# Optimization experiments

Measured on AMD Instinct MI355X. Metric: run time of the kernel, lower is better.

Reference implementation:

```python
import jax, jax.numpy as jnp
import numpy as np

B, S, D = 2, 2048, 2048
NQ, NKV = 32, 8
HD = D // NQ  # 64
THETA = 10000.0


def _rope_tables(seq_len, head_dim, theta):
    k = jnp.arange(0, head_dim, 2)[: head_dim // 2].astype(jnp.float32)
    inv_freq = 1.0 / (theta ** (k / head_dim))
    pos = jnp.arange(seq_len, dtype=jnp.float32)
    ang = pos[:, None] * inv_freq[None, :]          # [S, HD/2]
    ang = jnp.concatenate([ang, ang], axis=-1)       # [S, HD]
    return jnp.cos(ang), jnp.sin(ang)


def _apply_rope(x, cos, sin):
    # x: [B, H, S, HD]; cos/sin: [S, HD]
    h = x.shape[-1] // 2
    x1, x2 = x[..., :h], x[..., h:]
    rotated = jnp.concatenate([-x2, x1], axis=-1)
    return (x * cos[None, None] + rotated * sin[None, None]).astype(x.dtype)


def setup_inputs() -> dict:
    key = jax.random.key(0)
    ks = jax.random.split(key, 6)
    x = jax.random.normal(ks[0], (B, S, D), dtype=jnp.float32)
    attention_mask = jnp.ones((B, S), dtype=jnp.int32)
    Wq = jax.random.normal(ks[1], (NQ * HD, D), dtype=jnp.float32) * 0.02
    Wk = jax.random.normal(ks[2], (NKV * HD, D), dtype=jnp.float32) * 0.02
    Wv = jax.random.normal(ks[3], (NKV * HD, D), dtype=jnp.float32) * 0.02
    Wo = jax.random.normal(ks[4], (D, D), dtype=jnp.float32) * 0.02
    return {"x": x, "attention_mask": attention_mask,
            "Wq": Wq, "Wk": Wk, "Wv": Wv, "Wo": Wo}


def reference(x, attention_mask, Wq, Wk, Wv, Wo):
    b, s, d = x.shape
    # projections (nn.Linear: y = x @ W.T)
    q = jnp.einsum('bsd,od->bso', x, Wq).reshape(b, s, NQ, HD).transpose(0, 2, 1, 3)
    k = jnp.einsum('bsd,od->bso', x, Wk).reshape(b, s, NKV, HD).transpose(0, 2, 1, 3)
    v = jnp.einsum('bsd,od->bso', x, Wv).reshape(b, s, NKV, HD).transpose(0, 2, 1, 3)
    cos, sin = _rope_tables(s, HD, THETA)
    q = _apply_rope(q, cos, sin)
    k = _apply_rope(k, cos, sin)
    g = NQ // NKV
    k = jnp.repeat(k, g, axis=1)  # [b, NQ, s, HD]
    v = jnp.repeat(v, g, axis=1)
    attn = jnp.einsum('bhqd,bhkd->bhqk', q, k)
    causal = jnp.triu(jnp.ones((s, s), dtype=bool), k=1)
    attn = jnp.where(causal[None, None], -jnp.inf, attn)
    attn = jax.nn.softmax(attn / jnp.sqrt(jnp.float32(HD)), axis=-1)
    out = jnp.einsum('bhqk,bhkd->bhqd', attn, v)
    out = out.transpose(0, 2, 1, 3).reshape(b, s, d)
    return jnp.einsum('bsd,od->bso', out, Wo)
```

## Files before the change

### kernel.cpp

```cpp
#include <hip/hip_runtime.h>

#define B_   2
#define S_   2048
#define D_   2048
#define NQ_  32
#define NKV_ 8
#define HD_  64

typedef unsigned short u16;
typedef __bf16 bf16x8 __attribute__((ext_vector_type(8)));
typedef __bf16 bf16x4 __attribute__((ext_vector_type(4)));
typedef short  s16x4  __attribute__((ext_vector_type(4)));
typedef float  f32x4  __attribute__((ext_vector_type(4)));

#define GLB __attribute__((address_space(1)))
#define LDS __attribute__((address_space(3)))

__device__ inline u16 f2b(float f){
  union { float f; unsigned u; } v; v.f = f;
  unsigned r = (v.u + 0x7fffu + ((v.u >> 16) & 1u)) >> 16;
  return (u16)r;
}
__device__ inline float b2f(u16 b){
  union { unsigned u; float f; } v; v.u = ((unsigned)b) << 16;
  return v.f;
}

__device__ inline f32x4 mfma16(bf16x4 a, bf16x4 b, f32x4 c){
  union U { bf16x4 b; s16x4 s; };
  U ua, ub; ua.b = a; ub.b = b;
  return __builtin_amdgcn_mfma_f32_16x16x16bf16_1k(ua.s, ub.s, c, 0, 0, 0);
}

__device__ inline bf16x4 pack4(float p0, float p1, float p2, float p3){
  union { float f; unsigned u; } a, b, c, d;
  a.f = p0; b.f = p1; c.f = p2; d.f = p3;
  union { uint2 u; bf16x4 v; } r;
  r.u.x = (a.u >> 16) | (b.u & 0xffff0000u);
  r.u.y = (c.u >> 16) | (d.u & 0xffff0000u);
  return r.v;
}

__global__ void k_f2b_all(const float* __restrict__ x,  const float* __restrict__ wq,
                          const float* __restrict__ wk, const float* __restrict__ wv,
                          const float* __restrict__ wo,
                          u16* __restrict__ xb, u16* __restrict__ wqkvb, u16* __restrict__ wob){
  int i = blockIdx.x * blockDim.x + threadIdx.x;
  const float* src; u16* dst; int off;
  if (i < 2097152)      { src = x;  dst = xb;                  off = i; }
  else if (i < 3145728) { src = wq; dst = wqkvb;               off = i - 2097152; }
  else if (i < 3407872) { src = wk; dst = wqkvb + 2048*2048;   off = i - 3145728; }
  else if (i < 3670016) { src = wv; dst = wqkvb + 2560*2048;   off = i - 3407872; }
  else                  { src = wo; dst = wob;                 off = i - 3670016; }
  float4 f = ((const float4*)src)[off];
  uint2 pk;
  pk.x = (unsigned)f2b(f.x) | ((unsigned)f2b(f.y) << 16);
  pk.y = (unsigned)f2b(f.z) | ((unsigned)f2b(f.w) << 16);
  ((uint2*)dst)[off] = pk;
}

#define GEMM_CORE(K)                                                           \
  __shared__ __align__(16) u16 As[128*64];                                     \
  __shared__ __align__(16) u16 Bs[128*64];                                     \
  const int tid  = threadIdx.x;                                               \
  const int lane = tid & 63;                                                  \
  const int wave = tid >> 6;                                                  \
  const int wm = wave >> 1, wn = wave & 1;                                    \
  const int quad = lane >> 4, l16 = lane & 15;                                \
  const u16* Ab = A  + (size_t)blockIdx.y * 128 * (K);                        \
  const u16* Bb = Bm + (size_t)blockIdx.x * 128 * (K);                        \
  f32x4 acc[4][4];                                                            \
  for (int i = 0; i < 4; i++)                                                 \
    for (int j = 0; j < 4; j++) acc[i][j] = (f32x4){0.f, 0.f, 0.f, 0.f};      \
  const int R0 = wave * 32;                                                   \
  const int lr = lane >> 3;                                                   \
  const int gc = ((lane & 7) ^ lr) * 8;                                       \
  const int sk = l16 & 7;                                                     \
  for (int k0 = 0; k0 < (K); k0 += 64){                                       \
    __syncthreads();                                                          \
    _Pragma("unroll")                                                         \
    for (int m = 0; m < 4; m++){                                              \
      const u16* ga = Ab + (size_t)(R0 + m*8 + lr) * (K) + k0 + gc;           \
      const u16* gb = Bb + (size_t)(R0 + m*8 + lr) * (K) + k0 + gc;           \
      __builtin_amdgcn_global_load_lds((const GLB void*)ga, (LDS void*)&As[(R0 + m*8)*64], 16, 0, 0); \
      __builtin_amdgcn_global_load_lds((const GLB void*)gb, (LDS void*)&Bs[(R0 + m*8)*64], 16, 0, 0); \
    }                                                                          \
    __syncthreads();                                                          \
    bf16x8 af[4][2], bfr[4][2];                                               \
    _Pragma("unroll")                                                         \
    for (int i = 0; i < 4; i++)                                               \
      _Pragma("unroll")                                                       \
      for (int h = 0; h < 2; h++)                                             \
        af[i][h]  = *(const bf16x8*)&As[(wm*64 + i*16 + l16)*64 + (((h*4 + quad) ^ sk)*8)]; \
    _Pragma("unroll")                                                         \
    for (int j = 0; j < 4; j++)                                               \
      _Pragma("unroll")                                                       \
      for (int h = 0; h < 2; h++)                                             \
        bfr[j][h] = *(const bf16x8*)&Bs[(wn*64 + j*16 + l16)*64 + (((h*4 + quad) ^ sk)*8)]; \
    _Pragma("unroll")                                                         \
    for (int i = 0; i < 4; i++)                                               \
      _Pragma("unroll")                                                       \
      for (int j = 0; j < 4; j++){                                            \
        acc[i][j] = __builtin_amdgcn_mfma_f32_16x16x32_bf16(af[i][0], bfr[j][0], acc[i][j], 0, 0, 0); \
        acc[i][j] = __builtin_amdgcn_mfma_f32_16x16x32_bf16(af[i][1], bfr[j][1], acc[i][j], 0, 0, 0); \
      }                                                                        \
  }

#define QSCALE 0.18033688011112042f
__global__ __launch_bounds__(256, 3) void k_gemm_qkv(const u16* __restrict__ A,
                                                     const u16* __restrict__ Bm,
                                                     u16* __restrict__ qT,
                                                     u16* __restrict__ kT,
                                                     u16* __restrict__ vT){
  GEMM_CORE(2048)

  const int cb = blockIdx.x*128 + wn*64;

  if (cb < 2560){
    const bool isq = (cb < 2048);
    const int hh   = (isq ? cb : (cb - 2048)) >> 6;
    const int NH   = isq ? NQ_ : NKV_;
    u16* base      = isq ? qT : kT;
    const float sc = isq ? QSCALE : 1.0f;
    #pragma unroll
    for (int j = 0; j < 2; j++){
      const int d2 = j*16 + l16;
      const float invf = __expf(-(float)d2 * (9.210340371976184f / 32.0f));
      #pragma unroll
      for (int i = 0; i < 4; i++){
        const int row0 = blockIdx.y*128 + wm*64 + i*16 + quad*4;
        #pragma unroll
        for (int r = 0; r < 4; r++){
          const int row = row0 + r;
          const int s = row & (S_ - 1), b = row >> 11;
          float ang = (float)s * invf;
          float sn = __sinf(ang), cs = __cosf(ang);
          const float x1 = acc[i][j][r] * sc, x2 = acc[i][j+2][r] * sc;
          u16* drow = base + ((size_t)(b*NH + hh) * S_ + s) * 64;
          drow[d2]      = f2b(x1*cs - x2*sn);
          drow[d2 + 32] = f2b(x2*cs + x1*sn);
        }
      }
    }
  } else {
    const int fbase = cb - 2560;
    #pragma unroll
    for (int j = 0; j < 4; j++){
      const int f = fbase + j*16 + l16;
      const int kvh = f >> 6, d = f & 63;
      #pragma unroll
      for (int i = 0; i < 4; i++){
        const int row0 = blockIdx.y*128 + wm*64 + i*16 + quad*4;
        const int s0 = row0 & (S_ - 1), b = row0 >> 11;
        uint2 pk;
        pk.x = (unsigned)f2b(acc[i][j][0]) | ((unsigned)f2b(acc[i][j][1]) << 16);
        pk.y = (unsigned)f2b(acc[i][j][2]) | ((unsigned)f2b(acc[i][j][3]) << 16);
        *(uint2*)(vT + ((size_t)(b*NKV_ + kvh) * 64 + d) * S_ + s0) = pk;
      }
    }
  }
}

__global__ __launch_bounds__(256, 3) void k_gemm_bt(const u16* __restrict__ A,
                                                    const u16* __restrict__ Bm,
                                                    float* __restrict__ C,
                                                    int N){
  GEMM_CORE(2048)
  for (int i = 0; i < 4; i++){
    int row0 = blockIdx.y*128 + wm*64 + i*16 + quad*4;
    for (int j = 0; j < 4; j++){
      int col = blockIdx.x*128 + wn*64 + j*16 + l16;
      for (int r = 0; r < 4; r++)
        C[(size_t)(row0 + r) * N + col] = acc[i][j][r];
    }
  }
}

__global__ __launch_bounds__(256) void k_attn(const u16* __restrict__ qT,
                                              const u16* __restrict__ kT,
                                              const u16* __restrict__ vT,
                                              u16* __restrict__ P1,
                                              u16* __restrict__ P2,
                                              float* __restrict__ l1,
                                              float* __restrict__ l2){
  __shared__ __align__(16) u16 Ks[2][64*64];
  __shared__ __align__(16) u16 Vs[2][64*64];

  const int bid  = blockIdx.x;
  const int kvh  = bid & 7;
  const int b    = (bid >> 3) & 1;
  const int hq   = (bid >> 4) & 3;
  const int p    = (bid >> 6) & 7;
  const int half = bid >> 9;
  const int h    = kvh*4 + hq;
  const int lane = threadIdx.x & 63, w = threadIdx.x >> 6;
  const int quad = lane >> 4, l16 = lane & 15;

  const u16* Qh = qT + (size_t)(b*NQ_ + h)    * S_ * 64;
  const u16* Kh = kT + (size_t)(b*NKV_ + kvh) * S_ * 64;
  const u16* Vh = vT + (size_t)(b*NKV_ + kvh) * 64 * S_;

  const int rr = lane >> 3;
  const int gg = (lane & 7) ^ rr;
  const int R  = w * 16;

  auto stage = [&](int c, int buf){
    const int kb = c * 64;
    const u16* gk0 = Kh + (size_t)(kb + R + rr)     * 64 + gg*8;
    const u16* gk1 = Kh + (size_t)(kb + R + 8 + rr) * 64 + gg*8;
    const u16* gv0 = Vh + (size_t)(R + rr)     * S_ + kb + gg*8;
    const u16* gv1 = Vh + (size_t)(R + 8 + rr) * S_ + kb + gg*8;
    __builtin_amdgcn_global_load_lds((const GLB void*)gk0, (LDS void*)&Ks[buf][R*64],     16, 0, 0);
    __builtin_amdgcn_global_load_lds((const GLB void*)gk1, (LDS void*)&Ks[buf][(R+8)*64], 16, 0, 0);
    __builtin_amdgcn_global_load_lds((const GLB void*)gv0, (LDS void*)&Vs[buf][R*64],     16, 0, 0);
    __builtin_amdgcn_global_load_lds((const GLB void*)gv1, (LDS void*)&Vs[buf][(R+8)*64], 16, 0, 0);
  };

  const int sw    = l16 & 7;
  const int koff0 = ((quad    ) ^ sw) * 8;
  const int koff1 = ((quad + 4) ^ sw) * 8;
  int voff[4];
  #pragma unroll
  for (int t = 0; t < 4; t++)
    voff[t] = (((2*t + (quad >> 1)) ^ sw) * 8) + (quad & 1)*4;

  for (int ph = 0; ph < 2; ph++){
    int tile, c0, c1, slot;
    if (ph == 0){ tile = p;
      if (half == 0){ c0 = 0;      c1 = p + 1;     slot = 0; }
      else          { c0 = p + 1;  c1 = 2*p + 2;   slot = 1; }
    } else {      tile = 15 - p;
      if (half == 0){ c0 = 16 - p; c1 = 32 - 2*p;  slot = 1; }
      else          { c0 = 0;      c1 = 16 - p;    slot = 0; }
    }
    const int qb0 = 2*tile, qb1 = 2*tile + 1;
    const int qr0 = tile*128 + w*16 + l16;
    const int qr1 = qr0 + 64;
    const int nc  = c1 - c0;

    if (ph == 1) __syncthreads();
    stage(c0, 0);

    bf16x8 qf[2][2];
    qf[0][0] = *(const bf16x8*)(Qh + (size_t)qr0*64 + quad*8);
    qf[0][1] = *(const bf16x8*)(Qh + (size_t)qr0*64 + 32 + quad*8);
    qf[1][0] = *(const bf16x8*)(Qh + (size_t)qr1*64 + quad*8);
    qf[1][1] = *(const bf16x8*)(Qh + (size_t)qr1*64 + 32 + quad*8);

    f32x4 o[2][4];
    #pragma unroll
    for (int s = 0; s < 2; s++)
      for (int dt = 0; dt < 4; dt++) o[s][dt] = (f32x4){0.f, 0.f, 0.f, 0.f};
    float lrow[2] = {0.f, 0.f};

    for (int i = 0; i < nc; i++){
      const int c = c0 + i;
      const int buf = i & 1;
      __syncthreads();
      if (i + 1 < nc) stage(c + 1, buf^1);

      const bool act0  = (c <= qb0);
      const bool diag0 = (c == qb0);
      const bool diag1 = (c == qb1);
      const u16* Kb = &Ks[buf][0];
      const u16* Vb = &Vs[buf][0];

      bf16x4 pk[2][4];
      #pragma unroll
      for (int t = 0; t < 4; t++){
        const bool n0 = act0 && !(diag0 && t > w);
        const bool n1 = !(diag1 && t > w);
        if (!n0 && !n1) continue;
        const int rowb = (t*16 + l16)*64;
        bf16x8 ka0 = *(const bf16x8*)&Kb[rowb + koff0];
        bf16x8 ka1 = *(const bf16x8*)&Kb[rowb + koff1];
        #pragma unroll
        for (int s = 0; s < 2; s++){
          if (s == 0 ? !n0 : !n1) continue;
          f32x4 z = (f32x4){0.f, 0.f, 0.f, 0.f};
          z = __builtin_amdgcn_mfma_f32_16x16x32_bf16(ka0, qf[s][0], z, 0, 0, 0);
          z = __builtin_amdgcn_mfma_f32_16x16x32_bf16(ka1, qf[s][1], z, 0, 0, 0);
          if ((s == 0 ? diag0 : diag1) && t == w){
            #pragma unroll
            for (int r = 0; r < 4; r++)
              if (quad*4 + r > l16) z[r] = -1e30f;
          }
          float p0 = __builtin_amdgcn_exp2f(z[0]);
          float p1 = __builtin_amdgcn_exp2f(z[1]);
          float p2 = __builtin_amdgcn_exp2f(z[2]);
          float p3 = __builtin_amdgcn_exp2f(z[3]);
          lrow[s] += (p0 + p1) + (p2 + p3);
          pk[s][t] = pack4(p0, p1, p2, p3);
        }
      }

      #pragma unroll
      for (int dt = 0; dt < 4; dt++){
        const int rowb = (dt*16 + l16)*64;
        #pragma unroll
        for (int t = 0; t < 4; t++){
          const bool n0 = act0 && !(diag0 && t > w);
          const bool n1 = !(diag1 && t > w);
          if (!n0 && !n1) continue;
          bf16x4 va = *(const bf16x4*)&Vb[rowb + voff[t]];
          if (n0) o[0][dt] = mfma16(va, pk[0][t], o[0][dt]);
          if (n1) o[1][dt] = mfma16(va, pk[1][t], o[1][dt]);
        }
      }
    }

    u16*   Pd = slot ? P2 : P1;
    float* ld = slot ? l2 : l1;
    #pragma unroll
    for (int s = 0; s < 2; s++){
      float lsum = lrow[s];
      lsum += __shfl_xor(lsum, 16, 64);
      lsum += __shfl_xor(lsum, 32, 64);
      const int qrow = s ? qr1 : qr0;
      if (quad == 0) ld[(size_t)(b*S_ + qrow)*NQ_ + h] = lsum;
      u16* orow = Pd + (size_t)(b*S_ + qrow) * D_ + h*64;
      #pragma unroll
      for (int dt = 0; dt < 4; dt++){
        uint2 pkd;
        u16 e0 = f2b(o[s][dt][0]), e1 = f2b(o[s][dt][1]);
        u16 e2 = f2b(o[s][dt][2]), e3 = f2b(o[s][dt][3]);
        pkd.x = (unsigned)e0 | ((unsigned)e1 << 16);
        pkd.y = (unsigned)e2 | ((unsigned)e3 << 16);
        *(uint2*)(orow + dt*16 + quad*4) = pkd;
      }
    }
  }
}

__global__ void k_combine(const u16* __restrict__ P1, const u16* __restrict__ P2,
                          const float* __restrict__ l1, const float* __restrict__ l2,
                          u16* __restrict__ out){
  int i = blockIdx.x * blockDim.x + threadIdx.x;
  int e = i << 2;
  int li = (e >> 11)*NQ_ + ((e >> 6) & 31);
  float inv = 1.0f / (l1[li] + l2[li]);
  uint2 a = *(const uint2*)(P1 + e);
  uint2 bq = *(const uint2*)(P2 + e);
  float o0 = (b2f(a.x & 0xffff)  + b2f(bq.x & 0xffff))  * inv;
  float o1 = (b2f(a.x >> 16)     + b2f(bq.x >> 16))     * inv;
  float o2 = (b2f(a.y & 0xffff)  + b2f(bq.y & 0xffff))  * inv;
  float o3 = (b2f(a.y >> 16)     + b2f(bq.y >> 16))     * inv;
  uint2 pk;
  pk.x = (unsigned)f2b(o0) | ((unsigned)f2b(o1) << 16);
  pk.y = (unsigned)f2b(o2) | ((unsigned)f2b(o3) << 16);
  *(uint2*)(out + e) = pk;
}

extern "C" void kernel_launch(void* const* d_in, const int* in_sizes, int n_in,
                              void* d_out, int out_size, void* d_ws, size_t ws_size,
                              hipStream_t stream){
  const float* x  = (const float*)d_in[0];
  const float* Wq = (const float*)d_in[2];
  const float* Wk = (const float*)d_in[3];
  const float* Wv = (const float*)d_in[4];
  const float* Wo = (const float*)d_in[5];

  char* ws = (char*)d_ws;
  u16*   xb    = (u16*)(ws);
  u16*   wqkvb = (u16*)(ws + 16777216);
  u16*   wob   = (u16*)(ws + 29360128);
  u16*   qTp   = (u16*)(ws + 37748736);
  u16*   kTp   = (u16*)(ws + 54525952);
  u16*   vTp   = (u16*)(ws + 58720256);
  u16*   P1    = xb;
  u16*   P2    = (u16*)(ws + 62914560);
  float* l1    = (float*)(ws + 79691776);
  float* l2    = (float*)(ws + 80216064);
  u16*   attnOut = qTp;

  k_f2b_all<<<dim3(18432), 256, 0, stream>>>(x, Wq, Wk, Wv, Wo, xb, wqkvb, wob);

  k_gemm_qkv<<<dim3(24, 32), 256, 0, stream>>>(xb, wqkvb, qTp, kTp, vTp);

  k_attn<<<dim3(1024), 256, 0, stream>>>(qTp, kTp, vTp, P1, P2, l1, l2);

  k_combine<<<dim3(8192), 256, 0, stream>>>(P1, P2, l1, l2, attnOut);

  k_gemm_bt<<<dim3(16, 32), 256, 0, stream>>>(attnOut, wob, (float*)d_out, 2048);
}
```

Before: 309.7 us.

## Split attention into one tile per block with heaviest tiles first

The attention kernel used to pair a light and a heavy query tile inside each of 1024 blocks, each block running two phases. It now launches 2048 blocks, and each block handles a single 128-row query tile and one half of its causal key range. Block indices are ordered so the longest tiles (T=15 down to 0) are scheduled first, which should give a longest-first load balance and more blocks to fill the CUs. The V-offset precompute is moved inline and the bf16x4 type is replaced by s16x4 to drop the union casts. The cost is a Q-fragment reload and output write per block, and more blocks with short work at the tail.

```diff
diff --git a/kernel.cpp b/kernel.cpp
--- a/kernel.cpp
+++ b/kernel.cpp
@@ -9,7 +9,6 @@
 
 typedef unsigned short u16;
 typedef __bf16 bf16x8 __attribute__((ext_vector_type(8)));
-typedef __bf16 bf16x4 __attribute__((ext_vector_type(4)));
 typedef short  s16x4  __attribute__((ext_vector_type(4)));
 typedef float  f32x4  __attribute__((ext_vector_type(4)));
 
@@ -26,16 +25,14 @@
   return v.f;
 }
 
-__device__ inline f32x4 mfma16(bf16x4 a, bf16x4 b, f32x4 c){
-  union U { bf16x4 b; s16x4 s; };
-  U ua, ub; ua.b = a; ub.b = b;
-  return __builtin_amdgcn_mfma_f32_16x16x16bf16_1k(ua.s, ub.s, c, 0, 0, 0);
-}
-
-__device__ inline bf16x4 pack4(float p0, float p1, float p2, float p3){
+__device__ inline f32x4 mfma16(s16x4 a, s16x4 b, f32x4 c){
+  return __builtin_amdgcn_mfma_f32_16x16x16bf16_1k(a, b, c, 0, 0, 0);
+}
+
+__device__ inline s16x4 pack4(float p0, float p1, float p2, float p3){
   union { float f; unsigned u; } a, b, c, d;
   a.f = p0; b.f = p1; c.f = p2; d.f = p3;
-  union { uint2 u; bf16x4 v; } r;
+  union { uint2 u; s16x4 v; } r;
   r.u.x = (a.u >> 16) | (b.u & 0xffff0000u);
   r.u.y = (c.u >> 16) | (d.u & 0xffff0000u);
   return r.v;
@@ -190,8 +187,9 @@
   const int kvh  = bid & 7;
   const int b    = (bid >> 3) & 1;
   const int hq   = (bid >> 4) & 3;
-  const int p    = (bid >> 6) & 7;
-  const int half = bid >> 9;
+  const int j    = bid >> 6;
+  const int T    = 15 - (j >> 1);
+  const int half = j & 1;
   const int h    = kvh*4 + hq;
   const int lane = threadIdx.x & 63, w = threadIdx.x >> 6;
   const int quad = lane >> 4, l16 = lane & 15;
@@ -219,115 +217,102 @@
   const int sw    = l16 & 7;
   const int koff0 = ((quad    ) ^ sw) * 8;
   const int koff1 = ((quad + 4) ^ sw) * 8;
-  int voff[4];
+
+  const int qb0 = 2*T, qb1 = 2*T + 1;
+  const int qr0 = T*128 + w*16 + l16;
+  const int qr1 = qr0 + 64;
+  const int c0  = half ? (T + 1) : 0;
+  const int nc  = T + 1;
+
+  stage(c0, 0);
+
+  bf16x8 qf[2][2];
+  qf[0][0] = *(const bf16x8*)(Qh + (size_t)qr0*64 + quad*8);
+  qf[0][1] = *(const bf16x8*)(Qh + (size_t)qr0*64 + 32 + quad*8);
+  qf[1][0] = *(const bf16x8*)(Qh + (size_t)qr1*64 + quad*8);
+  qf[1][1] = *(const bf16x8*)(Qh + (size_t)qr1*64 + 32 + quad*8);
+
+  f32x4 o[2][4];
   #pragma unroll
-  for (int t = 0; t < 4; t++)
-    voff[t] = (((2*t + (quad >> 1)) ^ sw) * 8) + (quad & 1)*4;
-
-  for (int ph = 0; ph < 2; ph++){
-    int tile, c0, c1, slot;
-    if (ph == 0){ tile = p;
-      if (half == 0){ c0 = 0;      c1 = p + 1;     slot = 0; }
-      else          { c0 = p + 1;  c1 = 2*p + 2;   slot = 1; }
-    } else {      tile = 15 - p;
-      if (half == 0){ c0 = 16 - p; c1 = 32 - 2*p;  slot = 1; }
-      else          { c0 = 0;      c1 = 16 - p;    slot = 0; }
-    }
-    const int qb0 = 2*tile, qb1 = 2*tile + 1;
-    const int qr0 = tile*128 + w*16 + l16;
-    const int qr1 = qr0 + 64;
-    const int nc  = c1 - c0;
-
-    if (ph == 1) __syncthreads();
-    stage(c0, 0);
-
-    bf16x8 qf[2][2];
-    qf[0][0] = *(const bf16x8*)(Qh + (size_t)qr0*64 + quad*8);
-    qf[0][1] = *(const bf16x8*)(Qh + (size_t)qr0*64 + 32 + quad*8);
-    qf[1][0] = *(const bf16x8*)(Qh + (size_t)qr1*64 + quad*8);
-    qf[1][1] = *(const bf16x8*)(Qh + (size_t)qr1*64 + 32 + quad*8);
-
-    f32x4 o[2][4];
-    #pragma unroll
-    for (int s = 0; s < 2; s++)
-      for (int dt = 0; dt < 4; dt++) o[s][dt] = (f32x4){0.f, 0.f, 0.f, 0.f};
-    float lrow[2] = {0.f, 0.f};
-
-    for (int i = 0; i < nc; i++){
-      const int c = c0 + i;
-      const int buf = i & 1;
-      __syncthreads();
-      if (i + 1 < nc) stage(c + 1, buf^1);
-
-      const bool act0  = (c <= qb0);
-      const bool diag0 = (c == qb0);
-      const bool diag1 = (c == qb1);
-      const u16* Kb = &Ks[buf][0];
-      const u16* Vb = &Vs[buf][0];
-
-      bf16x4 pk[2][4];
+  for (int s = 0; s < 2; s++)
+    for (int dt = 0; dt < 4; dt++) o[s][dt] = (f32x4){0.f, 0.f, 0.f, 0.f};
+  float lrow[2] = {0.f, 0.f};
+
+  for (int i = 0; i < nc; i++){
+    const int c = c0 + i;
+    const int buf = i & 1;
+    __syncthreads();
+    if (i + 1 < nc) stage(c + 1, buf^1);
+
+    const bool act0  = (c <= qb0);
+    const bool diag0 = (c == qb0);
+    const bool diag1 = (c == qb1);
+    const u16* Kb = &Ks[buf][0];
+    const u16* Vb = &Vs[buf][0];
+
+    s16x4 pk[2][4];
+    #pragma unroll
+    for (int t = 0; t < 4; t++){
+      const bool n0 = act0 && !(diag0 && t > w);
+      const bool n1 = !(diag1 && t > w);
+      if (!n0 && !n1) continue;
+      const int rowb = (t*16 + l16)*64;
+      bf16x8 ka0 = *(const bf16x8*)&Kb[rowb + koff0];
+      bf16x8 ka1 = *(const bf16x8*)&Kb[rowb + koff1];
+      #pragma unroll
+      for (int s = 0; s < 2; s++){
+        if (s == 0 ? !n0 : !n1) continue;
+        f32x4 z = (f32x4){0.f, 0.f, 0.f, 0.f};
+        z = __builtin_amdgcn_mfma_f32_16x16x32_bf16(ka0, qf[s][0], z, 0, 0, 0);
+        z = __builtin_amdgcn_mfma_f32_16x16x32_bf16(ka1, qf[s][1], z, 0, 0, 0);
+        if ((s == 0 ? diag0 : diag1) && t == w){
+          #pragma unroll
+          for (int r = 0; r < 4; r++)
+            if (quad*4 + r > l16) z[r] = -1e30f;
+        }
+        float p0 = __builtin_amdgcn_exp2f(z[0]);
+        float p1 = __builtin_amdgcn_exp2f(z[1]);
+        float p2 = __builtin_amdgcn_exp2f(z[2]);
+        float p3 = __builtin_amdgcn_exp2f(z[3]);
+        lrow[s] += (p0 + p1) + (p2 + p3);
+        pk[s][t] = pack4(p0, p1, p2, p3);
+      }
+    }
+
+    #pragma unroll
+    for (int dt = 0; dt < 4; dt++){
+      const int rowb = (dt*16 + l16)*64;
       #pragma unroll
       for (int t = 0; t < 4; t++){
         const bool n0 = act0 && !(diag0 && t > w);
         const bool n1 = !(diag1 && t > w);
         if (!n0 && !n1) continue;
-        const int rowb = (t*16 + l16)*64;
-        bf16x8 ka0 = *(const bf16x8*)&Kb[rowb + koff0];
-        bf16x8 ka1 = *(const bf16x8*)&Kb[rowb + koff1];
-        #pragma unroll
-        for (int s = 0; s < 2; s++){
-          if (s == 0 ? !n0 : !n1) continue;
-          f32x4 z = (f32x4){0.f, 0.f, 0.f, 0.f};
-          z = __builtin_amdgcn_mfma_f32_16x16x32_bf16(ka0, qf[s][0], z, 0, 0, 0);
-          z = __builtin_amdgcn_mfma_f32_16x16x32_bf16(ka1, qf[s][1], z, 0, 0, 0);
-          if ((s == 0 ? diag0 : diag1) && t == w){
-            #pragma unroll
-            for (int r = 0; r < 4; r++)
-              if (quad*4 + r > l16) z[r] = -1e30f;
-          }
-          float p0 = __builtin_amdgcn_exp2f(z[0]);
-          float p1 = __builtin_amdgcn_exp2f(z[1]);
-          float p2 = __builtin_amdgcn_exp2f(z[2]);
-          float p3 = __builtin_amdgcn_exp2f(z[3]);
-          lrow[s] += (p0 + p1) + (p2 + p3);
-          pk[s][t] = pack4(p0, p1, p2, p3);
-        }
+        const int vo = (((2*t + (quad >> 1)) ^ sw) * 8) + (quad & 1)*4;
+        s16x4 va = *(const s16x4*)&Vb[rowb + vo];
+        if (n0) o[0][dt] = mfma16(va, pk[0][t], o[0][dt]);
+        if (n1) o[1][dt] = mfma16(va, pk[1][t], o[1][dt]);
       }
-
-      #pragma unroll
-      for (int dt = 0; dt < 4; dt++){
-        const int rowb = (dt*16 + l16)*64;
-        #pragma unroll
-        for (int t = 0; t < 4; t++){
-          const bool n0 = act0 && !(diag0 && t > w);
-          const bool n1 = !(diag1 && t > w);
-          if (!n0 && !n1) continue;
-          bf16x4 va = *(const bf16x4*)&Vb[rowb + voff[t]];
-          if (n0) o[0][dt] = mfma16(va, pk[0][t], o[0][dt]);
-          if (n1) o[1][dt] = mfma16(va, pk[1][t], o[1][dt]);
-        }
-      }
-    }
-
-    u16*   Pd = slot ? P2 : P1;
-    float* ld = slot ? l2 : l1;
-    #pragma unroll
-    for (int s = 0; s < 2; s++){
-      float lsum = lrow[s];
-      lsum += __shfl_xor(lsum, 16, 64);
-      lsum += __shfl_xor(lsum, 32, 64);
-      const int qrow = s ? qr1 : qr0;
-      if (quad == 0) ld[(size_t)(b*S_ + qrow)*NQ_ + h] = lsum;
-      u16* orow = Pd + (size_t)(b*S_ + qrow) * D_ + h*64;
-      #pragma unroll
-      for (int dt = 0; dt < 4; dt++){
-        uint2 pkd;
-        u16 e0 = f2b(o[s][dt][0]), e1 = f2b(o[s][dt][1]);
-        u16 e2 = f2b(o[s][dt][2]), e3 = f2b(o[s][dt][3]);
-        pkd.x = (unsigned)e0 | ((unsigned)e1 << 16);
-        pkd.y = (unsigned)e2 | ((unsigned)e3 << 16);
-        *(uint2*)(orow + dt*16 + quad*4) = pkd;
-      }
+    }
+  }
+
+  u16*   Pd = half ? P2 : P1;
+  float* ld = half ? l2 : l1;
+  #pragma unroll
+  for (int s = 0; s < 2; s++){
+    float lsum = lrow[s];
+    lsum += __shfl_xor(lsum, 16, 64);
+    lsum += __shfl_xor(lsum, 32, 64);
+    const int qrow = s ? qr1 : qr0;
+    if (quad == 0) ld[(size_t)(b*S_ + qrow)*NQ_ + h] = lsum;
+    u16* orow = Pd + (size_t)(b*S_ + qrow) * D_ + h*64;
+    #pragma unroll
+    for (int dt = 0; dt < 4; dt++){
+      uint2 pkd;
+      u16 e0 = f2b(o[s][dt][0]), e1 = f2b(o[s][dt][1]);
+      u16 e2 = f2b(o[s][dt][2]), e3 = f2b(o[s][dt][3]);
+      pkd.x = (unsigned)e0 | ((unsigned)e1 << 16);
+      pkd.y = (unsigned)e2 | ((unsigned)e3 << 16);
+      *(uint2*)(orow + dt*16 + quad*4) = pkd;
     }
   }
 }
@@ -377,7 +362,7 @@
 
   k_gemm_qkv<<<dim3(24, 32), 256, 0, stream>>>(xb, wqkvb, qTp, kTp, vTp);
 
-  k_attn<<<dim3(1024), 256, 0, stream>>>(qTp, kTp, vTp, P1, P2, l1, l2);
+  k_attn<<<dim3(2048), 256, 0, stream>>>(qTp, kTp, vTp, P1, P2, l1, l2);
 
   k_combine<<<dim3(8192), 256, 0, stream>>>(P1, P2, l1, l2, attnOut);
 
```

New measurement: 288.4 us. -6.9%, faster.
